# Performance work log

Hardware: AMD Instinct MI355X
Metric: run time of the kernel (lower is better)

The kernel has to match this reference:

```python
import jax, jax.numpy as jnp
import numpy as np

D = 384      # embedding_dim (module-level global)
H = 6        # num_heads
HD = D // H  # head_size = 64
T = 256      # block_size (tril buffer cap)
B = 128


def _layernorm(x, gamma, beta, eps=1e-5):
    mu = jnp.mean(x, axis=-1, keepdims=True)
    var = jnp.var(x, axis=-1, keepdims=True)
    return (x - mu) * jax.lax.rsqrt(var + eps) * gamma + beta


def setup_inputs() -> dict:
    key = jax.random.key(0)
    ks = jax.random.split(key, 12)
    s = 0.02
    return {
        "x":   jax.random.normal(ks[0], (B, T, D), jnp.float32),
        "Wq":  jax.random.normal(ks[1], (H, D, HD), jnp.float32) * s,
        "Wk":  jax.random.normal(ks[2], (H, D, HD), jnp.float32) * s,
        "Wv":  jax.random.normal(ks[3], (H, D, HD), jnp.float32) * s,
        "Wp":  jax.random.normal(ks[4], (D, D), jnp.float32) * s,
        "bp":  jnp.zeros((D,), jnp.float32),
        "W1":  jax.random.normal(ks[5], (D, 4 * D), jnp.float32) * s,
        "b1":  jnp.zeros((4 * D,), jnp.float32),
        "W2":  jax.random.normal(ks[6], (4 * D, D), jnp.float32) * s,
        "b2":  jnp.zeros((D,), jnp.float32),
        "g1":  jnp.ones((D,), jnp.float32),
        "be1": jnp.zeros((D,), jnp.float32),
        "g2":  jnp.ones((D,), jnp.float32),
        "be2": jnp.zeros((D,), jnp.float32),
    }


def reference(x, Wq, Wk, Wv, Wp, bp, W1, b1, W2, b2, g1, be1, g2, be2):
    Bsz, Tlen, C = x.shape
    # pre-LN self-attention
    h = _layernorm(x, g1, be1)
    q = jnp.einsum("btd,hdk->bhtk", h, Wq)
    k = jnp.einsum("bsd,hdk->bhsk", h, Wk)
    v = jnp.einsum("bsd,hdk->bhsk", h, Wv)
    # NOTE: source divides by sqrt(C)=sqrt(embedding_dim), not sqrt(head_size)
    scores = jnp.einsum("bhtk,bhsk->bhts", q, k) / jnp.sqrt(jnp.float32(C))
    causal = jnp.tril(jnp.ones((Tlen, Tlen), bool))
    scores = jnp.where(causal, scores, jnp.float32(-jnp.inf))
    attn = jax.nn.softmax(scores, axis=-1)          # dropout = identity (eval)
    o = jnp.einsum("bhts,bhsk->bhtk", attn, v)      # [B,H,T,HD]
    o = o.transpose(0, 2, 1, 3).reshape(Bsz, Tlen, C)  # concat heads
    sa = o @ Wp + bp
    x = x + sa
    # pre-LN feed-forward
    h2 = _layernorm(x, g2, be2)
    ff = jax.nn.relu(h2 @ W1 + b1) @ W2 + b2
    return x + ff
```

## Files before the change

### kernel.cpp

```cpp
#include <hip/hip_runtime.h>
#include <cstdint>
#include <cstddef>

#define D_   384
#define Hn   6
#define HDm  64
#define T_   256
#define B_   128
#define NROW (B_ * T_)

typedef __bf16  bf16x8 __attribute__((ext_vector_type(8)));
typedef float   f32x4  __attribute__((ext_vector_type(4)));
typedef const __attribute__((address_space(1))) void gvoid;
typedef __attribute__((address_space(3))) void lvoid;

__device__ inline uint32_t bf16rn(float f) {
  uint32_t u = __float_as_uint(f);
  return (u + 0x7FFFu + ((u >> 16) & 1u)) >> 16;
}

__global__ __launch_bounds__(128) void ln_kernel(const float* __restrict__ x,
                                                 const float* __restrict__ g,
                                                 const float* __restrict__ b,
                                                 uint16_t* __restrict__ out) {
  int row = blockIdx.x, tid = threadIdx.x;
  const float* xr = x + (size_t)row * D_;
  float v0 = xr[tid], v1 = xr[tid + 128], v2 = xr[tid + 256];
  float s  = v0 + v1 + v2;
  float ss = v0 * v0 + v1 * v1 + v2 * v2;
#pragma unroll
  for (int off = 32; off > 0; off >>= 1) {
    s  += __shfl_down(s, off);
    ss += __shfl_down(ss, off);
  }
  __shared__ float red[4];
  if ((tid & 63) == 0) { red[(tid >> 6) * 2] = s; red[(tid >> 6) * 2 + 1] = ss; }
  __syncthreads();
  float S = red[0] + red[2], SS = red[1] + red[3];
  float mu  = S * (1.0f / D_);
  float var = SS * (1.0f / D_) - mu * mu;
  float inv = rsqrtf(var + 1e-5f);
  uint16_t* orow = out + (size_t)row * D_;
  orow[tid]       = (uint16_t)bf16rn((v0 - mu) * inv * g[tid]       + b[tid]);
  orow[tid + 128] = (uint16_t)bf16rn((v1 - mu) * inv * g[tid + 128] + b[tid + 128]);
  orow[tid + 256] = (uint16_t)bf16rn((v2 - mu) * inv * g[tid + 256] + b[tid + 256]);
}

__global__ __launch_bounds__(256) void pack_qkv_w(const float* __restrict__ Wq,
                                                  const float* __restrict__ Wk,
                                                  const float* __restrict__ Wv,
                                                  uint16_t* __restrict__ Wo) {
  int idx = blockIdx.x * 256 + threadIdx.x;
  if (idx >= 1152 * D_) return;
  int col = idx / D_, d = idx % D_;
  int which = col / 384, c2 = col % 384;
  int h = c2 / HDm, k = c2 % HDm;
  const float* W = (which == 0) ? Wq : (which == 1) ? Wk : Wv;
  Wo[idx] = (uint16_t)bf16rn(W[((size_t)h * D_ + d) * HDm + k]);
}

__global__ __launch_bounds__(256) void pack_wt(const float* __restrict__ W,
                                               uint16_t* __restrict__ Wt,
                                               int K, int N) {
  int idx = blockIdx.x * 256 + threadIdx.x;
  if (idx >= K * N) return;
  int n = idx / K, k = idx % K;
  Wt[idx] = (uint16_t)bf16rn(W[(size_t)k * N + n]);
}

__global__ __launch_bounds__(256) void gemm_bf16(const uint16_t* __restrict__ A,
                                                 const uint16_t* __restrict__ Bt,
                                                 const float* __restrict__ bias,
                                                 const float* __restrict__ resid,
                                                 void* __restrict__ Cout,
                                                 int M, int N, int K,
                                                 int relu, int store_f32) {
  __shared__ uint16_t As[2][128 * 32];
  __shared__ uint16_t Bs[2][128 * 32];
  int tid = threadIdx.x;
  int bm = blockIdx.x * 128, bn = blockIdx.y * 128;
  int lane = tid & 63, wave = tid >> 6;
  int wm = (wave >> 1) << 6;
  int wn = (wave & 1) << 6;
  int lr = lane & 15;
  int q  = lane >> 4;
  int r0 = q << 2;
  int rd_off = (q ^ (lr & 3)) << 3;

  int c0 = tid,        row0 = c0 >> 2;
  int c1 = 256 + tid,  row1 = c1 >> 2;
  int g0 = ((c0 & 3) ^ (row0 & 3)) << 3;
  int g1 = ((c1 & 3) ^ (row1 & 3)) << 3;
  const uint16_t* ga0 = A  + (size_t)(bm + row0) * K + g0;
  const uint16_t* ga1 = A  + (size_t)(bm + row1) * K + g1;
  const uint16_t* gb0 = Bt + (size_t)(bn + row0) * K + g0;
  const uint16_t* gb1 = Bt + (size_t)(bn + row1) * K + g1;

  f32x4 acc[4][4];
  const f32x4 zero = {0.f, 0.f, 0.f, 0.f};
#pragma unroll
  for (int i = 0; i < 4; ++i)
#pragma unroll
    for (int j = 0; j < 4; ++j) acc[i][j] = zero;

  int nk = K >> 5;
  __builtin_amdgcn_global_load_lds((gvoid*)ga0, (lvoid*)((char*)As[0] + c0 * 16), 16, 0, 0);
  __builtin_amdgcn_global_load_lds((gvoid*)gb0, (lvoid*)((char*)Bs[0] + c0 * 16), 16, 0, 0);
  __builtin_amdgcn_global_load_lds((gvoid*)ga1, (lvoid*)((char*)As[0] + c1 * 16), 16, 0, 0);
  __builtin_amdgcn_global_load_lds((gvoid*)gb1, (lvoid*)((char*)Bs[0] + c1 * 16), 16, 0, 0);

  for (int i = 0; i < nk; ++i) {
    int cur = i & 1;
    __syncthreads();
    if (i + 1 < nk) {
      int nxt = cur ^ 1, ko = (i + 1) << 5;
      __builtin_amdgcn_global_load_lds((gvoid*)(ga0 + ko), (lvoid*)((char*)As[nxt] + c0 * 16), 16, 0, 0);
      __builtin_amdgcn_global_load_lds((gvoid*)(gb0 + ko), (lvoid*)((char*)Bs[nxt] + c0 * 16), 16, 0, 0);
      __builtin_amdgcn_global_load_lds((gvoid*)(ga1 + ko), (lvoid*)((char*)As[nxt] + c1 * 16), 16, 0, 0);
      __builtin_amdgcn_global_load_lds((gvoid*)(gb1 + ko), (lvoid*)((char*)Bs[nxt] + c1 * 16), 16, 0, 0);
    }

    bf16x8 af[4], bfr[4];
#pragma unroll
    for (int ii = 0; ii < 4; ++ii)
      af[ii] = *(const bf16x8*)&As[cur][(wm + ii * 16 + lr) * 32 + rd_off];
#pragma unroll
    for (int j = 0; j < 4; ++j)
      bfr[j] = *(const bf16x8*)&Bs[cur][(wn + j * 16 + lr) * 32 + rd_off];
#pragma unroll
    for (int ii = 0; ii < 4; ++ii)
#pragma unroll
      for (int j = 0; j < 4; ++j)
        acc[ii][j] = __builtin_amdgcn_mfma_f32_16x16x32_bf16(af[ii], bfr[j], acc[ii][j], 0, 0, 0);
  }

#pragma unroll
  for (int i = 0; i < 4; ++i) {
#pragma unroll
    for (int r = 0; r < 4; ++r) {
      int rr = bm + wm + i * 16 + r0 + r;
#pragma unroll
      for (int j = 0; j < 4; ++j) {
        int col = bn + wn + j * 16 + lr;
        float v = acc[i][j][r];
        if (bias)  v += bias[col];
        if (relu)  v = fmaxf(v, 0.0f);
        if (resid) v += resid[(size_t)rr * N + col];
        if (store_f32) ((float*)Cout)[(size_t)rr * N + col] = v;
        else           ((uint16_t*)Cout)[(size_t)rr * N + col] = (uint16_t)bf16rn(v);
      }
    }
  }
}

__global__ __launch_bounds__(256, 2) void attn_mfma(const uint16_t* __restrict__ qkv,
                                                    uint16_t* __restrict__ o) {
  __shared__ uint16_t Kt[64 * 72];
  __shared__ uint16_t Vt[64 * 72];
  __shared__ uint16_t Pb[4 * 64 * 72];
  int bh = blockIdx.x;
  int b = bh / Hn, h = bh % Hn;
  int tid = threadIdx.x;
  int lane = tid & 63, w = tid >> 6;
  int ln = lane & 15, q = lane >> 4;
  int kq = q * 8;
  int m0 = w * 64;
  const uint16_t* base = qkv + (size_t)b * T_ * 1152;

  bf16x8 af[4][2];
#pragma unroll
  for (int i = 0; i < 4; ++i)
#pragma unroll
    for (int ks = 0; ks < 2; ++ks)
      af[i][ks] = *(const bf16x8*)(base + (size_t)(m0 + i * 16 + ln) * 1152 + h * HDm + ks * 32 + kq);

  f32x4 o_[4][4], m_[4], l_[4];
  const f32x4 zero = {0.f, 0.f, 0.f, 0.f};
#pragma unroll
  for (int i = 0; i < 4; ++i) {
    m_[i] = {-1e30f, -1e30f, -1e30f, -1e30f};
    l_[i] = zero;
#pragma unroll
    for (int n = 0; n < 4; ++n) o_[i][n] = zero;
  }
  const float cs = 0.07362222f;

  for (int jt = 0; jt < 4; ++jt) {
    if (jt) __syncthreads();
#pragma unroll
    for (int t = 0; t < 2; ++t) {
      int c = t * 256 + tid;
      int s = c >> 3, d0 = (c & 7) << 3;
      *(uint4*)&Kt[s * 72 + d0] =
          *(const uint4*)(base + (size_t)(jt * 64 + s) * 1152 + 384 + h * HDm + d0);
    }
    {
      int sv = tid & 63, dv = (tid >> 6) << 4;
      const uint16_t* gv = base + (size_t)(jt * 64 + sv) * 1152 + 768 + h * HDm + dv;
      uint16_t tmp[16];
      *(uint4*)&tmp[0] = *(const uint4*)gv;
      *(uint4*)&tmp[8] = *(const uint4*)(gv + 8);
#pragma unroll
      for (int jj = 0; jj < 16; ++jj) Vt[(dv + jj) * 72 + sv] = tmp[jj];
    }
    __syncthreads();

    if (w >= jt) {
      f32x4 s2[4][4];
#pragma unroll
      for (int i = 0; i < 4; ++i)
#pragma unroll
        for (int j = 0; j < 4; ++j) s2[i][j] = zero;
#pragma unroll
      for (int ks = 0; ks < 2; ++ks) {
        bf16x8 bf[4];
#pragma unroll
        for (int j = 0; j < 4; ++j)
          bf[j] = *(const bf16x8*)&Kt[(j * 16 + ln) * 72 + ks * 32 + kq];
#pragma unroll
        for (int i = 0; i < 4; ++i)
#pragma unroll
          for (int j = 0; j < 4; ++j)
            s2[i][j] = __builtin_amdgcn_mfma_f32_16x16x32_bf16(af[i][ks], bf[j], s2[i][j], 0, 0, 0);
      }
#pragma unroll
      for (int i = 0; i < 4; ++i) {
#pragma unroll
        for (int j = 0; j < 4; ++j)
#pragma unroll
          for (int r = 0; r < 4; ++r) s2[i][j][r] *= cs;
        if (jt == w) {
#pragma unroll
          for (int j = 0; j < 4; ++j)
#pragma unroll
            for (int r = 0; r < 4; ++r)
              if (j * 16 + ln > i * 16 + q * 4 + r) s2[i][j][r] = -1e30f;
        }
        f32x4 rm;
#pragma unroll
        for (int r = 0; r < 4; ++r)
          rm[r] = fmaxf(fmaxf(s2[i][0][r], s2[i][1][r]), fmaxf(s2[i][2][r], s2[i][3][r]));
#pragma unroll
        for (int off = 1; off < 16; off <<= 1)
#pragma unroll
          for (int r = 0; r < 4; ++r)
            rm[r] = fmaxf(rm[r], __shfl_xor(rm[r], off));
        f32x4 mn, al, ps;
#pragma unroll
        for (int r = 0; r < 4; ++r) {
          mn[r] = fmaxf(m_[i][r], rm[r]);
          al[r] = exp2f(m_[i][r] - mn[r]);
          ps[r] = 0.f;
        }
        m_[i] = mn;
#pragma unroll
        for (int j = 0; j < 4; ++j)
#pragma unroll
          for (int r = 0; r < 4; ++r) {
            float p = exp2f(s2[i][j][r] - mn[r]);
            s2[i][j][r] = p;
            ps[r] += p;
          }
#pragma unroll
        for (int r = 0; r < 4; ++r) l_[i][r] = l_[i][r] * al[r] + ps[r];
#pragma unroll
        for (int n = 0; n < 4; ++n)
#pragma unroll
          for (int r = 0; r < 4; ++r) o_[i][n][r] *= al[r];
#pragma unroll
        for (int j = 0; j < 4; ++j)
#pragma unroll
          for (int r = 0; r < 4; ++r)
            Pb[w * 4608 + (i * 16 + q * 4 + r) * 72 + j * 16 + ln] =
                (uint16_t)bf16rn(s2[i][j][r]);
      }
      bf16x8 pa[4][2];
#pragma unroll
      for (int i = 0; i < 4; ++i)
#pragma unroll
        for (int ks = 0; ks < 2; ++ks)
          pa[i][ks] = *(const bf16x8*)&Pb[w * 4608 + (i * 16 + ln) * 72 + ks * 32 + kq];
#pragma unroll
      for (int n = 0; n < 4; ++n) {
        bf16x8 bv0 = *(const bf16x8*)&Vt[(n * 16 + ln) * 72 + kq];
        bf16x8 bv1 = *(const bf16x8*)&Vt[(n * 16 + ln) * 72 + 32 + kq];
#pragma unroll
        for (int i = 0; i < 4; ++i) {
          o_[i][n] = __builtin_amdgcn_mfma_f32_16x16x32_bf16(pa[i][0], bv0, o_[i][n], 0, 0, 0);
          o_[i][n] = __builtin_amdgcn_mfma_f32_16x16x32_bf16(pa[i][1], bv1, o_[i][n], 0, 0, 0);
        }
      }
    }
  }
#pragma unroll
  for (int i = 0; i < 4; ++i) {
    f32x4 lt = l_[i];
#pragma unroll
    for (int off = 1; off < 16; off <<= 1)
#pragma unroll
      for (int r = 0; r < 4; ++r) lt[r] += __shfl_xor(lt[r], off);
#pragma unroll
    for (int r = 0; r < 4; ++r) {
      float inv = 1.0f / lt[r];
      int row = b * T_ + m0 + i * 16 + q * 4 + r;
      uint16_t* op = o + (size_t)row * D_ + h * HDm;
#pragma unroll
      for (int n = 0; n < 4; ++n)
        op[n * 16 + ln] = (uint16_t)bf16rn(o_[i][n][r] * inv);
    }
  }
}

extern "C" void kernel_launch(void* const* d_in, const int* in_sizes, int n_in,
                              void* d_out, int out_size, void* d_ws, size_t ws_size,
                              hipStream_t stream) {
  const float* x   = (const float*)d_in[0];
  const float* Wq  = (const float*)d_in[1];
  const float* Wk  = (const float*)d_in[2];
  const float* Wv  = (const float*)d_in[3];
  const float* Wp  = (const float*)d_in[4];
  const float* bp  = (const float*)d_in[5];
  const float* W1  = (const float*)d_in[6];
  const float* b1  = (const float*)d_in[7];
  const float* W2  = (const float*)d_in[8];
  const float* b2  = (const float*)d_in[9];
  const float* g1  = (const float*)d_in[10];
  const float* be1 = (const float*)d_in[11];
  const float* g2  = (const float*)d_in[12];
  const float* be2 = (const float*)d_in[13];
  float* out = (float*)d_out;

  char* ws = (char*)d_ws;
  uint16_t* hbuf  = (uint16_t*)ws;
  uint16_t* qkv   = (uint16_t*)(ws + 25165824ull);
  uint16_t* ob    = (uint16_t*)(ws + 100663296ull);
  uint16_t* ff1   = qkv;
  uint16_t* Wqkvt = (uint16_t*)(ws + 125829120ull);
  uint16_t* Wpt   = (uint16_t*)(ws + 126713856ull);
  uint16_t* W1t   = (uint16_t*)(ws + 127008768ull);
  uint16_t* W2t   = (uint16_t*)(ws + 128188416ull);

  pack_qkv_w<<<(1152 * D_ + 255) / 256, 256, 0, stream>>>(Wq, Wk, Wv, Wqkvt);
  pack_wt<<<(384 * 384 + 255) / 256, 256, 0, stream>>>(Wp, Wpt, 384, 384);
  pack_wt<<<(384 * 1536 + 255) / 256, 256, 0, stream>>>(W1, W1t, 384, 1536);
  pack_wt<<<(1536 * 384 + 255) / 256, 256, 0, stream>>>(W2, W2t, 1536, 384);
  ln_kernel<<<NROW, 128, 0, stream>>>(x, g1, be1, hbuf);
  gemm_bf16<<<dim3(NROW / 128, 1152 / 128), 256, 0, stream>>>(
      hbuf, Wqkvt, nullptr, nullptr, qkv, NROW, 1152, 384, 0, 0);
  attn_mfma<<<B_ * Hn, 256, 0, stream>>>(qkv, ob);
  gemm_bf16<<<dim3(NROW / 128, 384 / 128), 256, 0, stream>>>(
      ob, Wpt, bp, x, out, NROW, 384, 384, 0, 1);
  ln_kernel<<<NROW, 128, 0, stream>>>(out, g2, be2, hbuf);
  gemm_bf16<<<dim3(NROW / 128, 1536 / 128), 256, 0, stream>>>(
      hbuf, W1t, b1, nullptr, ff1, NROW, 1536, 384, 1, 0);
  gemm_bf16<<<dim3(NROW / 128, 384 / 128), 256, 0, stream>>>(
      ff1, W2t, b2, out, out, NROW, 384, 1536, 0, 1);
}
```

Measured before the change: 520.2 us.

## Widen GEMM tile to 128x192 with k-major LDS layout

Raises the GEMM block tile from 128x128 to 128x192, giving each wave 64x96 outputs (24 MFMA accumulators). The shared-memory tiles move from a row-major XOR-swizzled layout to a k-chunk-major layout, so each 16-byte fragment read is contiguous by row within a k-group. The goal is more arithmetic per loaded byte and fewer blocks. In exchange it uses more registers per thread, asks for 2 blocks per CU, and produces fewer blocks for the N=384 GEMMs (2 column tiles instead of 3).

```diff
diff --git a/kernel.cpp b/kernel.cpp
--- a/kernel.cpp
+++ b/kernel.cpp
@@ -68,69 +68,72 @@
   Wt[idx] = (uint16_t)bf16rn(W[(size_t)k * N + n]);
 }
 
-__global__ __launch_bounds__(256) void gemm_bf16(const uint16_t* __restrict__ A,
-                                                 const uint16_t* __restrict__ Bt,
-                                                 const float* __restrict__ bias,
-                                                 const float* __restrict__ resid,
-                                                 void* __restrict__ Cout,
-                                                 int M, int N, int K,
-                                                 int relu, int store_f32) {
-  __shared__ uint16_t As[2][128 * 32];
-  __shared__ uint16_t Bs[2][128 * 32];
+__global__ __launch_bounds__(256, 2) void gemm_bf16(const uint16_t* __restrict__ A,
+                                                    const uint16_t* __restrict__ Bt,
+                                                    const float* __restrict__ bias,
+                                                    const float* __restrict__ resid,
+                                                    void* __restrict__ Cout,
+                                                    int M, int N, int K,
+                                                    int relu, int store_f32) {
+  __shared__ uint16_t As[2][4096];
+  __shared__ uint16_t Bs[2][6144];
   int tid = threadIdx.x;
-  int bm = blockIdx.x * 128, bn = blockIdx.y * 128;
+  int bm = blockIdx.x * 128, bn = blockIdx.y * 192;
   int lane = tid & 63, wave = tid >> 6;
   int wm = (wave >> 1) << 6;
-  int wn = (wave & 1) << 6;
+  int wn = (wave & 1) * 96;
   int lr = lane & 15;
   int q  = lane >> 4;
   int r0 = q << 2;
-  int rd_off = (q ^ (lr & 3)) << 3;
-
-  int c0 = tid,        row0 = c0 >> 2;
-  int c1 = 256 + tid,  row1 = c1 >> 2;
-  int g0 = ((c0 & 3) ^ (row0 & 3)) << 3;
-  int g1 = ((c1 & 3) ^ (row1 & 3)) << 3;
-  const uint16_t* ga0 = A  + (size_t)(bm + row0) * K + g0;
-  const uint16_t* ga1 = A  + (size_t)(bm + row1) * K + g1;
-  const uint16_t* gb0 = Bt + (size_t)(bn + row0) * K + g0;
-  const uint16_t* gb1 = Bt + (size_t)(bn + row1) * K + g1;
-
-  f32x4 acc[4][4];
+
+  int sA0 = tid,       rA0 = sA0 & 127, kA0 = sA0 >> 7;
+  int sA1 = 256 + tid, rA1 = sA1 & 127, kA1 = sA1 >> 7;
+  int sB0 = tid,       kB0 = sB0 / 192, rB0 = sB0 - kB0 * 192;
+  int sB1 = 256 + tid, kB1 = sB1 / 192, rB1 = sB1 - kB1 * 192;
+  int sB2 = 512 + tid, kB2 = sB2 / 192, rB2 = sB2 - kB2 * 192;
+  const uint16_t* gA0 = A  + (size_t)(bm + rA0) * K + kA0 * 8;
+  const uint16_t* gA1 = A  + (size_t)(bm + rA1) * K + kA1 * 8;
+  const uint16_t* gB0 = Bt + (size_t)(bn + rB0) * K + kB0 * 8;
+  const uint16_t* gB1 = Bt + (size_t)(bn + rB1) * K + kB1 * 8;
+  const uint16_t* gB2 = Bt + (size_t)(bn + rB2) * K + kB2 * 8;
+
+  f32x4 acc[4][6];
   const f32x4 zero = {0.f, 0.f, 0.f, 0.f};
 #pragma unroll
   for (int i = 0; i < 4; ++i)
 #pragma unroll
-    for (int j = 0; j < 4; ++j) acc[i][j] = zero;
+    for (int j = 0; j < 6; ++j) acc[i][j] = zero;
 
   int nk = K >> 5;
-  __builtin_amdgcn_global_load_lds((gvoid*)ga0, (lvoid*)((char*)As[0] + c0 * 16), 16, 0, 0);
-  __builtin_amdgcn_global_load_lds((gvoid*)gb0, (lvoid*)((char*)Bs[0] + c0 * 16), 16, 0, 0);
-  __builtin_amdgcn_global_load_lds((gvoid*)ga1, (lvoid*)((char*)As[0] + c1 * 16), 16, 0, 0);
-  __builtin_amdgcn_global_load_lds((gvoid*)gb1, (lvoid*)((char*)Bs[0] + c1 * 16), 16, 0, 0);
+  __builtin_amdgcn_global_load_lds((gvoid*)gA0, (lvoid*)((char*)As[0] + sA0 * 16), 16, 0, 0);
+  __builtin_amdgcn_global_load_lds((gvoid*)gA1, (lvoid*)((char*)As[0] + sA1 * 16), 16, 0, 0);
+  __builtin_amdgcn_global_load_lds((gvoid*)gB0, (lvoid*)((char*)Bs[0] + sB0 * 16), 16, 0, 0);
+  __builtin_amdgcn_global_load_lds((gvoid*)gB1, (lvoid*)((char*)Bs[0] + sB1 * 16), 16, 0, 0);
+  __builtin_amdgcn_global_load_lds((gvoid*)gB2, (lvoid*)((char*)Bs[0] + sB2 * 16), 16, 0, 0);
 
   for (int i = 0; i < nk; ++i) {
     int cur = i & 1;
     __syncthreads();
     if (i + 1 < nk) {
       int nxt = cur ^ 1, ko = (i + 1) << 5;
-      __builtin_amdgcn_global_load_lds((gvoid*)(ga0 + ko), (lvoid*)((char*)As[nxt] + c0 * 16), 16, 0, 0);
-      __builtin_amdgcn_global_load_lds((gvoid*)(gb0 + ko), (lvoid*)((char*)Bs[nxt] + c0 * 16), 16, 0, 0);
-      __builtin_amdgcn_global_load_lds((gvoid*)(ga1 + ko), (lvoid*)((char*)As[nxt] + c1 * 16), 16, 0, 0);
-      __builtin_amdgcn_global_load_lds((gvoid*)(gb1 + ko), (lvoid*)((char*)Bs[nxt] + c1 * 16), 16, 0, 0);
-    }
-
-    bf16x8 af[4], bfr[4];
+      __builtin_amdgcn_global_load_lds((gvoid*)(gA0 + ko), (lvoid*)((char*)As[nxt] + sA0 * 16), 16, 0, 0);
+      __builtin_amdgcn_global_load_lds((gvoid*)(gA1 + ko), (lvoid*)((char*)As[nxt] + sA1 * 16), 16, 0, 0);
+      __builtin_amdgcn_global_load_lds((gvoid*)(gB0 + ko), (lvoid*)((char*)Bs[nxt] + sB0 * 16), 16, 0, 0);
+      __builtin_amdgcn_global_load_lds((gvoid*)(gB1 + ko), (lvoid*)((char*)Bs[nxt] + sB1 * 16), 16, 0, 0);
+      __builtin_amdgcn_global_load_lds((gvoid*)(gB2 + ko), (lvoid*)((char*)Bs[nxt] + sB2 * 16), 16, 0, 0);
+    }
+
+    bf16x8 af[4], bfr[6];
 #pragma unroll
     for (int ii = 0; ii < 4; ++ii)
-      af[ii] = *(const bf16x8*)&As[cur][(wm + ii * 16 + lr) * 32 + rd_off];
-#pragma unroll
-    for (int j = 0; j < 4; ++j)
-      bfr[j] = *(const bf16x8*)&Bs[cur][(wn + j * 16 + lr) * 32 + rd_off];
+      af[ii] = *(const bf16x8*)&As[cur][(q * 128 + wm + ii * 16 + lr) * 8];
+#pragma unroll
+    for (int j = 0; j < 6; ++j)
+      bfr[j] = *(const bf16x8*)&Bs[cur][(q * 192 + wn + j * 16 + lr) * 8];
 #pragma unroll
     for (int ii = 0; ii < 4; ++ii)
 #pragma unroll
-      for (int j = 0; j < 4; ++j)
+      for (int j = 0; j < 6; ++j)
         acc[ii][j] = __builtin_amdgcn_mfma_f32_16x16x32_bf16(af[ii], bfr[j], acc[ii][j], 0, 0, 0);
   }
 
@@ -140,7 +143,7 @@
     for (int r = 0; r < 4; ++r) {
       int rr = bm + wm + i * 16 + r0 + r;
 #pragma unroll
-      for (int j = 0; j < 4; ++j) {
+      for (int j = 0; j < 6; ++j) {
         int col = bn + wn + j * 16 + lr;
         float v = acc[i][j][r];
         if (bias)  v += bias[col];
@@ -345,14 +348,14 @@
   pack_wt<<<(384 * 1536 + 255) / 256, 256, 0, stream>>>(W1, W1t, 384, 1536);
   pack_wt<<<(1536 * 384 + 255) / 256, 256, 0, stream>>>(W2, W2t, 1536, 384);
   ln_kernel<<<NROW, 128, 0, stream>>>(x, g1, be1, hbuf);
-  gemm_bf16<<<dim3(NROW / 128, 1152 / 128), 256, 0, stream>>>(
+  gemm_bf16<<<dim3(NROW / 128, 1152 / 192), 256, 0, stream>>>(
       hbuf, Wqkvt, nullptr, nullptr, qkv, NROW, 1152, 384, 0, 0);
   attn_mfma<<<B_ * Hn, 256, 0, stream>>>(qkv, ob);
-  gemm_bf16<<<dim3(NROW / 128, 384 / 128), 256, 0, stream>>>(
+  gemm_bf16<<<dim3(NROW / 128, 384 / 192), 256, 0, stream>>>(
       ob, Wpt, bp, x, out, NROW, 384, 384, 0, 1);
   ln_kernel<<<NROW, 128, 0, stream>>>(out, g2, be2, hbuf);
-  gemm_bf16<<<dim3(NROW / 128, 1536 / 128), 256, 0, stream>>>(
+  gemm_bf16<<<dim3(NROW / 128, 1536 / 192), 256, 0, stream>>>(
       hbuf, W1t, b1, nullptr, ff1, NROW, 1536, 384, 1, 0);
-  gemm_bf16<<<dim3(NROW / 128, 384 / 128), 256, 0, stream>>>(
+  gemm_bf16<<<dim3(NROW / 128, 384 / 192), 256, 0, stream>>>(
       ff1, W2t, b2, out, out, NROW, 384, 1536, 0, 1);
 }
```

New measurement: 614.3 us. 1.18x slower.
